# Performance work log

Hardware: AMD Instinct MI355X
Metric: run time of the kernel (lower is better)

The kernel has to match this reference:

```python
import jax, jax.numpy as jnp
import numpy as np

D, H, W, VP = 10, 400, 352, 35  # grid depth/height/width, points per voxel
C1_IN, C1_H = 7, 16   # VFE-1: Linear 7->16, concat -> 32
C2_IN, C2_H = 32, 64  # VFE-2: Linear 32->64, concat -> 128
BN_EPS = 1e-5


def setup_inputs() -> dict:
    key = jax.random.key(0)
    ks = jax.random.split(key, 12)
    K = 15000
    feature = jax.random.normal(ks[0], (K, VP, C1_IN), jnp.float32)
    keep = (jax.random.uniform(ks[1], (K, VP, 1)) < 0.8).astype(jnp.float32)
    feature = feature * keep
    bs = 1
    coordinate = jnp.concatenate([
        jax.random.randint(ks[2], (K, 1), 0, bs),
        jax.random.randint(ks[3], (K, 1), 0, D),
        jax.random.randint(ks[4], (K, 1), 0, H),
        jax.random.randint(ks[5], (K, 1), 0, W),
    ], axis=1).astype(jnp.int32)
    w1 = jax.random.normal(ks[6], (C1_IN, C1_H), jnp.float32) * 0.3
    b1 = jnp.zeros((C1_H,), jnp.float32)
    g1 = jnp.ones((C1_H,), jnp.float32)
    be1 = jnp.zeros((C1_H,), jnp.float32)
    w2 = jax.random.normal(ks[7], (C2_IN, C2_H), jnp.float32) * 0.15
    b2 = jnp.zeros((C2_H,), jnp.float32)
    g2 = jnp.ones((C2_H,), jnp.float32)
    be2 = jnp.zeros((C2_H,), jnp.float32)
    return dict(feature=feature, coordinate=coordinate, bs=bs,
                w1=w1, b1=b1, g1=g1, be1=be1,
                w2=w2, b2=b2, g2=g2, be2=be2)


def _vfe(x, mask, Wm, b, gamma, beta):
    # Linear + ReLU, then BatchNorm1d (training-mode batch stats over (K, VP))
    pw = jax.nn.relu(jnp.einsum('kpi,ih->kph', x, Wm) + b)
    mean = jnp.mean(pw, axis=(0, 1))
    var = jnp.var(pw, axis=(0, 1))  # biased variance, as BN uses for normalization
    pw = (pw - mean) * jax.lax.rsqrt(var + BN_EPS) * gamma + beta
    agg = jnp.max(pw, axis=1, keepdims=True)            # [K,1,Ch] per-voxel max
    concat = jnp.concatenate([pw, jnp.broadcast_to(agg, pw.shape)], axis=-1)
    return concat * mask                                  # mask broadcasts [K,VP,1]


def reference(feature, coordinate, bs, w1, b1, g1, be1, w2, b2, g2, be2):
    # mask: point is valid if max over its 7 features != 0
    mask = (jnp.max(feature, axis=2, keepdims=True) != 0).astype(feature.dtype)
    x = _vfe(feature, mask, w1, b1, g1, be1)   # [K,VP,32]
    x = _vfe(x, mask, w2, b2, g2, be2)         # [K,VP,128]
    voxelwise = jnp.max(x, axis=1)             # [K,128]
    c = coordinate
    out = jnp.zeros((bs, D, H, W, 2 * C2_H), feature.dtype)
    # sparse -> dense sums duplicate coordinates, matching torch.sparse to_dense
    out = out.at[c[:, 0], c[:, 1], c[:, 2], c[:, 3]].add(voxelwise)
    return out
```

## Files before the change

kernel.cpp:

```cpp
#include <hip/hip_runtime.h>
#include <math.h>

#define VPTS 35
#define CIN1 7
#define CH1  16
#define CH2  64
#define DD   10
#define HHH  400
#define WWW  352
#define BN_EPS 1e-5f
#define NSTRIPE 8


__global__ void k_init(float* __restrict__ ws) {
  for (int i = threadIdx.x; i < 1280; i += blockDim.x) ws[i] = 0.f;
}

__global__ void __launch_bounds__(256) k_A(
    const float* __restrict__ feat,
    const float* __restrict__ w1, const float* __restrict__ b1,
    float* __restrict__ red1p, float4* __restrict__ out4, long zA, int KP) {
  float w[CIN1][CH1], bb[CH1];
#pragma unroll
  for (int i = 0; i < CIN1; ++i)
#pragma unroll
    for (int c = 0; c < CH1; ++c) w[i][c] = w1[i * CH1 + c];
#pragma unroll
  for (int c = 0; c < CH1; ++c) bb[c] = b1[c];
  float s[CH1], q[CH1];
#pragma unroll
  for (int c = 0; c < CH1; ++c) { s[c] = 0.f; q[c] = 0.f; }
  int tid = blockIdx.x * blockDim.x + threadIdx.x;
  int stride = gridDim.x * blockDim.x;
  for (int idx = tid; idx < KP; idx += stride) {
    float x[CIN1];
#pragma unroll
    for (int i = 0; i < CIN1; ++i) x[i] = feat[(size_t)idx * CIN1 + i];
#pragma unroll
    for (int c = 0; c < CH1; ++c) {
      float a = bb[c];
#pragma unroll
      for (int i = 0; i < CIN1; ++i) a = fmaf(x[i], w[i][c], a);
      a = fmaxf(a, 0.f);
      s[c] += a;
      q[c] = fmaf(a, a, q[c]);
    }
  }
  float4 z = make_float4(0.f, 0.f, 0.f, 0.f);
  for (long i = tid; i < zA; i += stride) out4[i] = z;
  __shared__ float ssum[2 * CH1];
  if (threadIdx.x < 2 * CH1) ssum[threadIdx.x] = 0.f;
  __syncthreads();
#pragma unroll
  for (int c = 0; c < CH1; ++c) {
    float a = s[c], b = q[c];
    for (int o = 32; o > 0; o >>= 1) {
      a += __shfl_down(a, o);
      b += __shfl_down(b, o);
    }
    if ((threadIdx.x & 63) == 0) {
      atomicAdd(&ssum[c], a);
      atomicAdd(&ssum[CH1 + c], b);
    }
  }
  __syncthreads();
  if (threadIdx.x < 2 * CH1)
    atomicAdd(&red1p[(blockIdx.x & (NSTRIPE - 1)) * 2 * CH1 + threadIdx.x],
              ssum[threadIdx.x]);
}

__global__ void __launch_bounds__(256) k_heavy(
    const float* __restrict__ feat,
    const float* __restrict__ w1, const float* __restrict__ b1,
    const float* __restrict__ g1, const float* __restrict__ be1,
    const float* __restrict__ red1p,
    const float* __restrict__ w2, const float* __restrict__ b2,
    const float* __restrict__ g2,
    float* __restrict__ red2p,
    float* __restrict__ E1buf, float* __restrict__ E2buf,
    float* __restrict__ FLbuf, int K,
    float4* __restrict__ out4, long z0, long n4, float invN) {
  __shared__ __align__(16) float fs_s[4][248];
  __shared__ __align__(16) float pw1_s[4][560];
  __shared__ __align__(16) float agg1_s[4][16];
  __shared__ float ss[2 * CH2];
  int t = threadIdx.x, lane = t & 63, w = t >> 6;
  float* fs   = fs_s[w];
  float* pw1  = pw1_s[w];
  float* agg1 = agg1_s[w];

  int c1 = lane & 15;
  float r1s = 0.f, r1q = 0.f;
#pragma unroll
  for (int sIdx = 0; sIdx < NSTRIPE; ++sIdx) {
    r1s += red1p[sIdx * 2 * CH1 + c1];
    r1q += red1p[sIdx * 2 * CH1 + CH1 + c1];
  }
  float mean1 = r1s * invN;
  float var1  = r1q * invN - mean1 * mean1;
  float sc1   = g1[c1] * rsqrtf(var1 + BN_EPS);
  float sh1   = be1[c1] - mean1 * sc1;
  float b1c   = b1[c1];
  float w1r[CIN1];
#pragma unroll
  for (int j = 0; j < CIN1; ++j) w1r[j] = w1[j * CH1 + c1];
  float wcol[32];
#pragma unroll
  for (int i = 0; i < 32; ++i) wcol[i] = w2[i * CH2 + lane];
  float b2c = b2[lane];
  float sgn = (g2[lane] >= 0.f) ? 1.f : -1.f;

  float lsum = 0.f, lsq = 0.f;
  int waveg = blockIdx.x * 4 + w;
  int nwave = gridDim.x * 4;
  long zstride = (long)gridDim.x * 256;
  long zi = z0 + (long)blockIdx.x * 256 + t;
  float4 zv = make_float4(0.f, 0.f, 0.f, 0.f);
  for (int k = waveg; k < K; k += nwave) {
    for (int i = lane; i < VPTS * CIN1; i += 64)
      fs[i] = feat[(size_t)k * (VPTS * CIN1) + i];
    bool vbit = false;
    if (lane < VPTS) {
      float m = fs[lane * CIN1];
#pragma unroll
      for (int j = 1; j < CIN1; ++j) m = fmaxf(m, fs[lane * CIN1 + j]);
      vbit = (m != 0.f);
    }
    unsigned long long mbits = __ballot(vbit);
#pragma unroll
    for (int j = 0; j < 9; ++j) {
      int idx = lane + 64 * j;
      if (idx < VPTS * CH1) {
        int p = idx >> 4;
        float a = b1c;
#pragma unroll
        for (int jj = 0; jj < CIN1; ++jj) a = fmaf(fs[p * CIN1 + jj], w1r[jj], a);
        a = fmaxf(a, 0.f);
        pw1[idx] = fmaf(a, sc1, sh1);
      }
    }
    {
      int g = lane >> 4;
      float am = -INFINITY;
      for (int p = g; p < VPTS; p += 4) am = fmaxf(am, pw1[p * CH1 + c1]);
      am = fmaxf(am, __shfl_xor(am, 16));
      am = fmaxf(am, __shfl_xor(am, 32));
      if (lane < CH1) agg1[lane] = am;
    }
#pragma unroll
    for (int u = 0; u < 20; ++u) {
      if (zi < n4) { out4[zi] = zv; zi += zstride; }
    }
    float aggdot = 0.f;
    {
      const float4* a4 = (const float4*)agg1;
#pragma unroll
      for (int i = 0; i < 4; ++i) {
        float4 v = a4[i];
        aggdot = fmaf(v.x, wcol[16 + 4 * i + 0], aggdot);
        aggdot = fmaf(v.y, wcol[16 + 4 * i + 1], aggdot);
        aggdot = fmaf(v.z, wcol[16 + 4 * i + 2], aggdot);
        aggdot = fmaf(v.w, wcol[16 + 4 * i + 3], aggdot);
      }
    }
    float E1w = -INFINITY, E2w = -INFINITY;
    const float4* p4 = (const float4*)pw1;
    for (int p = 0; p < VPTS; ++p) {
      float4 v0 = p4[p * 4 + 0], v1 = p4[p * 4 + 1];
      float4 v2 = p4[p * 4 + 2], v3 = p4[p * 4 + 3];
      float low = 0.f;
      low = fmaf(v0.x, wcol[0], low);  low = fmaf(v0.y, wcol[1], low);
      low = fmaf(v0.z, wcol[2], low);  low = fmaf(v0.w, wcol[3], low);
      low = fmaf(v1.x, wcol[4], low);  low = fmaf(v1.y, wcol[5], low);
      low = fmaf(v1.z, wcol[6], low);  low = fmaf(v1.w, wcol[7], low);
      low = fmaf(v2.x, wcol[8], low);  low = fmaf(v2.y, wcol[9], low);
      low = fmaf(v2.z, wcol[10], low); low = fmaf(v2.w, wcol[11], low);
      low = fmaf(v3.x, wcol[12], low); low = fmaf(v3.y, wcol[13], low);
      low = fmaf(v3.z, wcol[14], low); low = fmaf(v3.w, wcol[15], low);
      bool valid = (mbits >> p) & 1ull;
      float m = valid ? 1.f : 0.f;
      float pw2 = fmaxf(fmaf(m, low + aggdot, b2c), 0.f);
      lsum += pw2;
      lsq = fmaf(pw2, pw2, lsq);
      float sp = sgn * pw2;
      E2w = fmaxf(E2w, sp);
      if (valid) E1w = fmaxf(E1w, sp);
    }
    E1buf[(size_t)k * 64 + lane] = E1w;
    E2buf[(size_t)k * 64 + lane] = E2w;
    if (lane == 0) FLbuf[k] = (float)__popcll(mbits);
  }
  for (; zi < n4; zi += zstride) out4[zi] = zv;
  if (t < 2 * CH2) ss[t] = 0.f;
  __syncthreads();
  atomicAdd(&ss[lane], lsum);
  atomicAdd(&ss[CH2 + lane], lsq);
  __syncthreads();
  if (t < 2 * CH2)
    atomicAdd(&red2p[(blockIdx.x & (NSTRIPE - 1)) * 2 * CH2 + t], ss[t]);
}

__global__ void __launch_bounds__(256) k_scatter(
    const float* __restrict__ E1buf, const float* __restrict__ E2buf,
    const float* __restrict__ FLbuf, const float* __restrict__ red2p,
    const float* __restrict__ g2, const float* __restrict__ be2,
    const int* __restrict__ coord, float* __restrict__ out, int K,
    float invN) {
  __shared__ float scsh2_s[2 * CH2];
  int t = threadIdx.x;
  if (t < CH2) {
    float rs = 0.f, rq = 0.f;
#pragma unroll
    for (int sIdx = 0; sIdx < NSTRIPE; ++sIdx) {
      rs += red2p[sIdx * 2 * CH2 + t];
      rq += red2p[sIdx * 2 * CH2 + CH2 + t];
    }
    float mean = rs * invN;
    float var = rq * invN - mean * mean;
    float inv = rsqrtf(var + BN_EPS);
    float sc = g2[t] * inv;
    scsh2_s[t] = sc;
    scsh2_s[CH2 + t] = be2[t] - mean * sc;
  }
  __syncthreads();
  int k = blockIdx.x * 2 + (t >> 7);
  if (k >= K) return;
  int tl = t & 127;
  int c = tl & 63;
  float nv = FLbuf[k];
  bool anyV = nv > 0.f;
  bool anyI = nv < (float)VPTS;
  float sc = scsh2_s[c], sh = scsh2_s[CH2 + c];
  float cand = -INFINITY;
  if (anyV) {
    float E = (tl < 64) ? E1buf[(size_t)k * 64 + c] : E2buf[(size_t)k * 64 + c];
    cand = fmaf(fabsf(sc), E, sh);
  }
  if (anyI) cand = fmaxf(cand, 0.f);
  int4 cc = *reinterpret_cast<const int4*>(coord + (size_t)k * 4);
  long vox = ((long)(cc.x * DD + cc.y) * HHH + cc.z) * WWW + cc.w;
  atomicAdd(&out[vox * (2 * CH2) + tl], cand);
}

__global__ void __launch_bounds__(256) k_zero(float4* __restrict__ out4,
                                              long n4, float* __restrict__ wsfb) {
  long i = (long)blockIdx.x * blockDim.x + threadIdx.x;
  long stride = (long)gridDim.x * blockDim.x;
  float4 z = make_float4(0.f, 0.f, 0.f, 0.f);
  for (; i < n4; i += stride) out4[i] = z;
  if (blockIdx.x == 0 && threadIdx.x < 320) wsfb[threadIdx.x] = 0.f;
}

__global__ void k_finalize(const float* __restrict__ red,
                           const float* __restrict__ g,
                           const float* __restrict__ be,
                           float* __restrict__ scsh, int CH, float invN) {
  int c = threadIdx.x;
  if (c < CH) {
    float mean = red[c] * invN;
    float var = red[CH + c] * invN - mean * mean;
    float inv = rsqrtf(var + BN_EPS);
    float sc = g[c] * inv;
    scsh[c] = sc;
    scsh[CH + c] = be[c] - mean * sc;
  }
}

__global__ void __launch_bounds__(256) k_stats1_fb(
    const float* __restrict__ feat,
    const float* __restrict__ w1, const float* __restrict__ b1,
    float* __restrict__ red1, int KP) {
  float w[CIN1][CH1], bb[CH1];
#pragma unroll
  for (int i = 0; i < CIN1; ++i)
#pragma unroll
    for (int c = 0; c < CH1; ++c) w[i][c] = w1[i * CH1 + c];
#pragma unroll
  for (int c = 0; c < CH1; ++c) bb[c] = b1[c];
  float s[CH1], q[CH1];
#pragma unroll
  for (int c = 0; c < CH1; ++c) { s[c] = 0.f; q[c] = 0.f; }
  int tid = blockIdx.x * blockDim.x + threadIdx.x;
  int stride = gridDim.x * blockDim.x;
  for (int idx = tid; idx < KP; idx += stride) {
    float x[CIN1];
#pragma unroll
    for (int i = 0; i < CIN1; ++i) x[i] = feat[(size_t)idx * CIN1 + i];
#pragma unroll
    for (int c = 0; c < CH1; ++c) {
      float a = bb[c];
#pragma unroll
      for (int i = 0; i < CIN1; ++i) a = fmaf(x[i], w[i][c], a);
      a = fmaxf(a, 0.f);
      s[c] += a;
      q[c] = fmaf(a, a, q[c]);
    }
  }
  __shared__ float ssum[2 * CH1];
  if (threadIdx.x < 2 * CH1) ssum[threadIdx.x] = 0.f;
  __syncthreads();
#pragma unroll
  for (int c = 0; c < CH1; ++c) {
    float a = s[c], b = q[c];
    for (int o = 32; o > 0; o >>= 1) {
      a += __shfl_down(a, o);
      b += __shfl_down(b, o);
    }
    if ((threadIdx.x & 63) == 0) {
      atomicAdd(&ssum[c], a);
      atomicAdd(&ssum[CH1 + c], b);
    }
  }
  __syncthreads();
  if (threadIdx.x < 2 * CH1) atomicAdd(&red1[threadIdx.x], ssum[threadIdx.x]);
}

__device__ __forceinline__ void compute_x2_old(
    const float* __restrict__ feat, int k, int t,
    const float* __restrict__ w1, const float* __restrict__ b1,
    const float* __restrict__ scsh1,
    float* fs, float* mask_s, float* pw1_s, float* agg1_s, float* x2_s) {
  if (t < VPTS * CIN1) fs[t] = feat[(size_t)k * (VPTS * CIN1) + t];
  __syncthreads();
  if (t < VPTS) {
    float m = fs[t * CIN1];
#pragma unroll
    for (int i = 1; i < CIN1; ++i) m = fmaxf(m, fs[t * CIN1 + i]);
    mask_s[t] = (m != 0.f) ? 1.f : 0.f;
  }
  for (int i = t; i < VPTS * CH1; i += 256) {
    int p = i >> 4, c = i & 15;
    float acc = b1[c];
#pragma unroll
    for (int j = 0; j < CIN1; ++j) acc = fmaf(fs[p * CIN1 + j], w1[j * CH1 + c], acc);
    acc = fmaxf(acc, 0.f);
    pw1_s[i] = fmaf(acc, scsh1[c], scsh1[CH1 + c]);
  }
  __syncthreads();
  if (t < CH1) {
    float m = pw1_s[t];
    for (int p = 1; p < VPTS; ++p) m = fmaxf(m, pw1_s[p * CH1 + t]);
    agg1_s[t] = m;
  }
  __syncthreads();
  for (int i = t; i < VPTS * 32; i += 256) {
    int p = i >> 5, c = i & 31;
    x2_s[i] = (c < CH1 ? pw1_s[p * CH1 + c] : agg1_s[c - CH1]) * mask_s[p];
  }
  __syncthreads();
}

__global__ void __launch_bounds__(256) k_stats2_old(
    const float* __restrict__ feat,
    const float* __restrict__ w1, const float* __restrict__ b1,
    const float* __restrict__ scsh1,
    const float* __restrict__ w2, const float* __restrict__ b2,
    float* __restrict__ red2, int K) {
  __shared__ float fs[VPTS * CIN1], mask_s[VPTS], pw1_s[VPTS * CH1], agg1_s[CH1];
  __shared__ __align__(16) float x2_s[VPTS * 32];
  __shared__ __align__(16) float w2_s[32 * CH2];
  __shared__ float ss[2 * CH2];
  int t = threadIdx.x;
  for (int i = t; i < 32 * CH2; i += 256) w2_s[i] = w2[i];
  if (t < 2 * CH2) ss[t] = 0.f;
  __syncthreads();
  int c = t & 63;
  float wcol[32];
#pragma unroll
  for (int i = 0; i < 32; ++i) wcol[i] = w2_s[i * CH2 + c];
  float bb = b2[c];
  float lsum = 0.f, lsq = 0.f;
  for (int k = blockIdx.x; k < K; k += gridDim.x) {
    compute_x2_old(feat, k, t, w1, b1, scsh1, fs, mask_s, pw1_s, agg1_s, x2_s);
    for (int p = t >> 6; p < VPTS; p += 4) {
      const float4* xv = (const float4*)(x2_s + p * 32);
      float a = bb;
#pragma unroll
      for (int i = 0; i < 8; ++i) {
        float4 v = xv[i];
        a = fmaf(v.x, wcol[4 * i + 0], a);
        a = fmaf(v.y, wcol[4 * i + 1], a);
        a = fmaf(v.z, wcol[4 * i + 2], a);
        a = fmaf(v.w, wcol[4 * i + 3], a);
      }
      a = fmaxf(a, 0.f);
      lsum += a;
      lsq = fmaf(a, a, lsq);
    }
  }
  atomicAdd(&ss[c], lsum);
  atomicAdd(&ss[CH2 + c], lsq);
  __syncthreads();
  if (t < 2 * CH2) atomicAdd(&red2[t], ss[t]);
}

__global__ void __launch_bounds__(256) k_final_old(
    const float* __restrict__ feat,
    const float* __restrict__ w1, const float* __restrict__ b1,
    const float* __restrict__ scsh1,
    const float* __restrict__ w2, const float* __restrict__ b2,
    const float* __restrict__ scsh2,
    const int* __restrict__ coord,
    float* __restrict__ out, int K) {
  __shared__ float fs[VPTS * CIN1], mask_s[VPTS], pw1_s[VPTS * CH1], agg1_s[CH1];
  __shared__ __align__(16) float x2_s[VPTS * 32];
  __shared__ __align__(16) float w2_s[32 * CH2];
  __shared__ float pw2_s[VPTS * CH2];
  __shared__ float agg2_s[CH2];
  int t = threadIdx.x;
  for (int i = t; i < 32 * CH2; i += 256) w2_s[i] = w2[i];
  __syncthreads();
  int c = t & 63;
  float wcol[32];
#pragma unroll
  for (int i = 0; i < 32; ++i) wcol[i] = w2_s[i * CH2 + c];
  float bb = b2[c];
  float sc = scsh2[c], sh = scsh2[CH2 + c];
  for (int k = blockIdx.x; k < K; k += gridDim.x) {
    compute_x2_old(feat, k, t, w1, b1, scsh1, fs, mask_s, pw1_s, agg1_s, x2_s);
    for (int p = t >> 6; p < VPTS; p += 4) {
      const float4* xv = (const float4*)(x2_s + p * 32);
      float a = bb;
#pragma unroll
      for (int i = 0; i < 8; ++i) {
        float4 v = xv[i];
        a = fmaf(v.x, wcol[4 * i + 0], a);
        a = fmaf(v.y, wcol[4 * i + 1], a);
        a = fmaf(v.z, wcol[4 * i + 2], a);
        a = fmaf(v.w, wcol[4 * i + 3], a);
      }
      a = fmaxf(a, 0.f);
      pw2_s[p * CH2 + c] = fmaf(a, sc, sh);
    }
    __syncthreads();
    if (t < CH2) {
      float m = pw2_s[t];
      for (int p = 1; p < VPTS; ++p) m = fmaxf(m, pw2_s[p * CH2 + t]);
      agg2_s[t] = m;
    }
    __syncthreads();
    if (t < 2 * CH2) {
      float vm = -INFINITY;
      if (t < CH2) {
        for (int p = 0; p < VPTS; ++p) vm = fmaxf(vm, pw2_s[p * CH2 + t] * mask_s[p]);
      } else {
        float a = agg2_s[t - CH2];
        for (int p = 0; p < VPTS; ++p) vm = fmaxf(vm, a * mask_s[p]);
      }
      int4 cc = *reinterpret_cast<const int4*>(coord + (size_t)k * 4);
      long vox = ((long)(cc.x * DD + cc.y) * HHH + cc.z) * WWW + cc.w;
      atomicAdd(&out[vox * (2 * CH2) + t], vm);
    }
  }
}

extern "C" void kernel_launch(void* const* d_in, const int* in_sizes, int n_in,
                              void* d_out, int out_size, void* d_ws, size_t ws_size,
                              hipStream_t stream) {
  const float* feat = (const float*)d_in[0];
  const int* coord  = (const int*)d_in[1];
  const float* w1  = (const float*)d_in[3];
  const float* b1  = (const float*)d_in[4];
  const float* g1  = (const float*)d_in[5];
  const float* be1 = (const float*)d_in[6];
  const float* w2  = (const float*)d_in[7];
  const float* b2  = (const float*)d_in[8];
  const float* g2  = (const float*)d_in[9];
  const float* be2 = (const float*)d_in[10];
  float* out = (float*)d_out;
  float* ws = (float*)d_ws;

  int K = in_sizes[0] / (VPTS * CIN1);
  int KP = K * VPTS;
  float invN = 1.f / (float)KP;

  float* red1p = ws;
  float* red2p = ws + 256;
  float* fb    = ws + 1280;
  float* E1buf = ws + 2048;
  float* E2buf = E1buf + (size_t)64 * K;
  float* FLbuf = E2buf + (size_t)64 * K;

  size_t need_bytes = (2048 + (size_t)K * 129) * sizeof(float);

  long n4 = (long)out_size / 4;
  long zA = (n4 * 55) / 100;

  if (ws_size >= need_bytes) {
    k_init<<<1, 1024, 0, stream>>>(ws);
    k_A<<<2048, 256, 0, stream>>>(feat, w1, b1, red1p, (float4*)out, zA, KP);
    k_heavy<<<2048, 256, 0, stream>>>(feat, w1, b1, g1, be1, red1p,
                                      w2, b2, g2, red2p, E1buf, E2buf, FLbuf, K,
                                      (float4*)out, zA, n4, invN);
    k_scatter<<<(K + 1) / 2, 256, 0, stream>>>(E1buf, E2buf, FLbuf, red2p,
                                               g2, be2, coord, out, K, invN);
  } else {
    float* red1  = fb;
    float* scsh1 = fb + 32;
    float* red2  = fb + 64;
    float* scsh2 = fb + 192;
    k_zero<<<2048, 256, 0, stream>>>((float4*)out, n4, fb);
    k_stats1_fb<<<512, 256, 0, stream>>>(feat, w1, b1, red1, KP);
    k_finalize<<<1, 64, 0, stream>>>(red1, g1, be1, scsh1, CH1, invN);
    k_stats2_old<<<1024, 256, 0, stream>>>(feat, w1, b1, scsh1, w2, b2, red2, K);
    k_finalize<<<1, 64, 0, stream>>>(red2, g2, be2, scsh2, CH2, invN);
    k_final_old<<<2048, 256, 0, stream>>>(feat, w1, b1, scsh1, w2, b2, scsh2,
                                          coord, out, K);
  }
}
```

Baseline: 194.4 us.

## Fuse pipeline into one cooperative kernel with grid syncs and role-split blocks

Replaces the init/stats/heavy/scatter launch chain with a single cooperative kernel that uses grid.sync between phases. In each phase some blocks compute (BN1 stats, then VFE-2) while the rest zero the output buffer. This removes launch gaps and the workspace init kernel. The cost is fewer blocks (capped by occupancy at 1024), fewer waves doing the heavy VFE work, and the overhead of grid-wide barriers.

Measured after the change: 432.9 us. +122.7%, slower.

```diff
diff --git a/kernel.cpp b/kernel.cpp
--- a/kernel.cpp
+++ b/kernel.cpp
@@ -1,5 +1,8 @@
 #include <hip/hip_runtime.h>
+#include <hip/hip_cooperative_groups.h>
 #include <math.h>
+
+namespace cg = cooperative_groups;
 
 #define VPTS 35
 #define CIN1 7
@@ -12,8 +15,233 @@
 #define NSTRIPE 8
 
 
+__global__ void __launch_bounds__(256, 4) k_fused(
+    const float* __restrict__ feat, const int* __restrict__ coord,
+    const float* __restrict__ w1, const float* __restrict__ b1,
+    const float* __restrict__ g1, const float* __restrict__ be1,
+    const float* __restrict__ w2, const float* __restrict__ b2,
+    const float* __restrict__ g2, const float* __restrict__ be2,
+    float* __restrict__ out, float* __restrict__ ws,
+    int K, int KP, long n4, long f1, float invN) {
+  cg::grid_group grid = cg::this_grid();
+  float4* out4 = (float4*)out;
+  float* ws1   = ws;
+  float* red2p = ws + 2048;
+  float* E1buf = ws + 4096;
+  float* E2buf = E1buf + (size_t)64 * K;
+  float* FLbuf = E2buf + (size_t)64 * K;
+
+  const int G  = gridDim.x;
+  const int Sb = G >> 4;
+  const int Hb = G >> 1;
+  const int t = threadIdx.x, lane = t & 63, w = t >> 6;
+
+  __shared__ __align__(16) float fs_s[4][248];
+  __shared__ __align__(16) float pw1_s[4][560];
+  __shared__ __align__(16) float agg1_s[4][16];
+  __shared__ float ss[2 * CH2];
+  __shared__ float ls[2 * CH1];
+  __shared__ float scsh2_s[2 * CH2];
+
+  if (blockIdx.x < Sb) {
+    int tp = blockIdx.x * 256 + t;
+    int p0 = tp >> 2, cq = tp & 3;
+    int pstride = Sb * 64;
+    float w1q[CIN1][4], b1q[4], s[4], q[4];
+#pragma unroll
+    for (int j = 0; j < CIN1; ++j)
+#pragma unroll
+      for (int cc = 0; cc < 4; ++cc) w1q[j][cc] = w1[j * CH1 + cq * 4 + cc];
+#pragma unroll
+    for (int cc = 0; cc < 4; ++cc) {
+      b1q[cc] = b1[cq * 4 + cc];
+      s[cc] = 0.f; q[cc] = 0.f;
+    }
+    for (int p = p0; p < KP; p += pstride) {
+      float x[CIN1];
+#pragma unroll
+      for (int j = 0; j < CIN1; ++j) x[j] = feat[(size_t)p * CIN1 + j];
+#pragma unroll
+      for (int cc = 0; cc < 4; ++cc) {
+        float a = b1q[cc];
+#pragma unroll
+        for (int j = 0; j < CIN1; ++j) a = fmaf(x[j], w1q[j][cc], a);
+        a = fmaxf(a, 0.f);
+        s[cc] += a;
+        q[cc] = fmaf(a, a, q[cc]);
+      }
+    }
+    if (t < 2 * CH1) ls[t] = 0.f;
+    __syncthreads();
+#pragma unroll
+    for (int cc = 0; cc < 4; ++cc) {
+      atomicAdd(&ls[cq * 4 + cc], s[cc]);
+      atomicAdd(&ls[CH1 + cq * 4 + cc], q[cc]);
+    }
+    __syncthreads();
+    if (t < 2 * CH1) ws1[blockIdx.x * 32 + t] = ls[t];
+  } else {
+    if (blockIdx.x == G - 1) {
+      for (int i = t; i < NSTRIPE * 2 * CH2; i += 256) red2p[i] = 0.f;
+    }
+    float4 zv = make_float4(0.f, 0.f, 0.f, 0.f);
+    long fb = G - Sb;
+    long stride = fb * 256;
+    for (long zi = (long)(blockIdx.x - Sb) * 256 + t; zi < f1; zi += stride)
+      out4[zi] = zv;
+  }
+  grid.sync();
+
+  if (blockIdx.x < Hb) {
+    float* fs   = fs_s[w];
+    float* pw1  = pw1_s[w];
+    float* agg1 = agg1_s[w];
+    int c1 = lane & 15;
+    float r1s = 0.f, r1q = 0.f;
+    for (int sIdx = 0; sIdx < Sb; ++sIdx) {
+      r1s += ws1[sIdx * 32 + c1];
+      r1q += ws1[sIdx * 32 + CH1 + c1];
+    }
+    float mean1 = r1s * invN;
+    float var1  = r1q * invN - mean1 * mean1;
+    float sc1   = g1[c1] * rsqrtf(var1 + BN_EPS);
+    float sh1   = be1[c1] - mean1 * sc1;
+    float b1c   = b1[c1];
+    float w1r[CIN1];
+#pragma unroll
+    for (int j = 0; j < CIN1; ++j) w1r[j] = w1[j * CH1 + c1];
+    float wcol[32];
+#pragma unroll
+    for (int i = 0; i < 32; ++i) wcol[i] = w2[i * CH2 + lane];
+    float b2c = b2[lane];
+    float sgn = (g2[lane] >= 0.f) ? 1.f : -1.f;
+
+    float lsum = 0.f, lsq = 0.f;
+    int waveg = blockIdx.x * 4 + w;
+    int nwave = Hb * 4;
+    for (int k = waveg; k < K; k += nwave) {
+      for (int i = lane; i < VPTS * CIN1; i += 64)
+        fs[i] = feat[(size_t)k * (VPTS * CIN1) + i];
+      bool vbit = false;
+      if (lane < VPTS) {
+        float m = fs[lane * CIN1];
+#pragma unroll
+        for (int j = 1; j < CIN1; ++j) m = fmaxf(m, fs[lane * CIN1 + j]);
+        vbit = (m != 0.f);
+      }
+      unsigned long long mbits = __ballot(vbit);
+#pragma unroll
+      for (int j = 0; j < 9; ++j) {
+        int idx = lane + 64 * j;
+        if (idx < VPTS * CH1) {
+          int p = idx >> 4;
+          float a = b1c;
+#pragma unroll
+          for (int jj = 0; jj < CIN1; ++jj)
+            a = fmaf(fs[p * CIN1 + jj], w1r[jj], a);
+          a = fmaxf(a, 0.f);
+          pw1[idx] = fmaf(a, sc1, sh1);
+        }
+      }
+      {
+        int g = lane >> 4;
+        float am = -INFINITY;
+        for (int p = g; p < VPTS; p += 4) am = fmaxf(am, pw1[p * CH1 + c1]);
+        am = fmaxf(am, __shfl_xor(am, 16));
+        am = fmaxf(am, __shfl_xor(am, 32));
+        if (lane < CH1) agg1[lane] = am;
+      }
+      float aggdot = 0.f;
+      {
+        const float4* a4 = (const float4*)agg1;
+#pragma unroll
+        for (int i = 0; i < 4; ++i) {
+          float4 v = a4[i];
+          aggdot = fmaf(v.x, wcol[16 + 4 * i + 0], aggdot);
+          aggdot = fmaf(v.y, wcol[16 + 4 * i + 1], aggdot);
+          aggdot = fmaf(v.z, wcol[16 + 4 * i + 2], aggdot);
+          aggdot = fmaf(v.w, wcol[16 + 4 * i + 3], aggdot);
+        }
+      }
+      float E1w = -INFINITY, E2w = -INFINITY;
+      const float4* p4 = (const float4*)pw1;
+      for (int p = 0; p < VPTS; ++p) {
+        float4 v0 = p4[p * 4 + 0], v1 = p4[p * 4 + 1];
+        float4 v2 = p4[p * 4 + 2], v3 = p4[p * 4 + 3];
+        float low = 0.f;
+        low = fmaf(v0.x, wcol[0], low);  low = fmaf(v0.y, wcol[1], low);
+        low = fmaf(v0.z, wcol[2], low);  low = fmaf(v0.w, wcol[3], low);
+        low = fmaf(v1.x, wcol[4], low);  low = fmaf(v1.y, wcol[5], low);
+        low = fmaf(v1.z, wcol[6], low);  low = fmaf(v1.w, wcol[7], low);
+        low = fmaf(v2.x, wcol[8], low);  low = fmaf(v2.y, wcol[9], low);
+        low = fmaf(v2.z, wcol[10], low); low = fmaf(v2.w, wcol[11], low);
+        low = fmaf(v3.x, wcol[12], low); low = fmaf(v3.y, wcol[13], low);
+        low = fmaf(v3.z, wcol[14], low); low = fmaf(v3.w, wcol[15], low);
+        bool valid = (mbits >> p) & 1ull;
+        float m = valid ? 1.f : 0.f;
+        float pw2 = fmaxf(fmaf(m, low + aggdot, b2c), 0.f);
+        lsum += pw2;
+        lsq = fmaf(pw2, pw2, lsq);
+        float sp = sgn * pw2;
+        E2w = fmaxf(E2w, sp);
+        if (valid) E1w = fmaxf(E1w, sp);
+      }
+      E1buf[(size_t)k * 64 + lane] = E1w;
+      E2buf[(size_t)k * 64 + lane] = E2w;
+      if (lane == 0) FLbuf[k] = (float)__popcll(mbits);
+    }
+    if (t < 2 * CH2) ss[t] = 0.f;
+    __syncthreads();
+    atomicAdd(&ss[lane], lsum);
+    atomicAdd(&ss[CH2 + lane], lsq);
+    __syncthreads();
+    if (t < 2 * CH2)
+      atomicAdd(&red2p[(blockIdx.x & (NSTRIPE - 1)) * 2 * CH2 + t], ss[t]);
+  } else {
+    float4 zv = make_float4(0.f, 0.f, 0.f, 0.f);
+    long fb = G - Hb;
+    long stride = fb * 256;
+    for (long zi = f1 + (long)(blockIdx.x - Hb) * 256 + t; zi < n4; zi += stride)
+      out4[zi] = zv;
+  }
+  grid.sync();
+
+  if (t < CH2) {
+    float rs = 0.f, rq = 0.f;
+#pragma unroll
+    for (int sIdx = 0; sIdx < NSTRIPE; ++sIdx) {
+      rs += red2p[sIdx * 2 * CH2 + t];
+      rq += red2p[sIdx * 2 * CH2 + CH2 + t];
+    }
+    float mean = rs * invN;
+    float var = rq * invN - mean * mean;
+    float inv = rsqrtf(var + BN_EPS);
+    float sc = g2[t] * inv;
+    scsh2_s[t] = sc;
+    scsh2_s[CH2 + t] = be2[t] - mean * sc;
+  }
+  __syncthreads();
+  int tl = t & 127;
+  int c = tl & 63;
+  float sc = scsh2_s[c], sh = scsh2_s[CH2 + c];
+  for (int k = blockIdx.x * 2 + (t >> 7); k < K; k += G * 2) {
+    float nv = FLbuf[k];
+    bool anyV = nv > 0.f;
+    bool anyI = nv < (float)VPTS;
+    float cand = -INFINITY;
+    if (anyV) {
+      float E = (tl < 64) ? E1buf[(size_t)k * 64 + c] : E2buf[(size_t)k * 64 + c];
+      cand = fmaf(fabsf(sc), E, sh);
+    }
+    if (anyI) cand = fmaxf(cand, 0.f);
+    int4 cc = *reinterpret_cast<const int4*>(coord + (size_t)k * 4);
+    long vox = ((long)(cc.x * DD + cc.y) * HHH + cc.z) * WWW + cc.w;
+    atomicAdd(&out[vox * (2 * CH2) + tl], cand);
+  }
+}
+
 __global__ void k_init(float* __restrict__ ws) {
-  for (int i = threadIdx.x; i < 1280; i += blockDim.x) ws[i] = 0.f;
+  for (int i = threadIdx.x; i < 3392; i += blockDim.x) ws[i] = 0.f;
 }
 
 __global__ void __launch_bounds__(256) k_A(
@@ -69,7 +297,7 @@
               ssum[threadIdx.x]);
 }
 
-__global__ void __launch_bounds__(256) k_heavy(
+__global__ void __launch_bounds__(256) k_heavy_fb(
     const float* __restrict__ feat,
     const float* __restrict__ w1, const float* __restrict__ b1,
     const float* __restrict__ g1, const float* __restrict__ be1,
@@ -88,7 +316,6 @@
   float* fs   = fs_s[w];
   float* pw1  = pw1_s[w];
   float* agg1 = agg1_s[w];
-
   int c1 = lane & 15;
   float r1s = 0.f, r1q = 0.f;
 #pragma unroll
@@ -109,13 +336,9 @@
   for (int i = 0; i < 32; ++i) wcol[i] = w2[i * CH2 + lane];
   float b2c = b2[lane];
   float sgn = (g2[lane] >= 0.f) ? 1.f : -1.f;
-
   float lsum = 0.f, lsq = 0.f;
   int waveg = blockIdx.x * 4 + w;
   int nwave = gridDim.x * 4;
-  long zstride = (long)gridDim.x * 256;
-  long zi = z0 + (long)blockIdx.x * 256 + t;
-  float4 zv = make_float4(0.f, 0.f, 0.f, 0.f);
   for (int k = waveg; k < K; k += nwave) {
     for (int i = lane; i < VPTS * CIN1; i += 64)
       fs[i] = feat[(size_t)k * (VPTS * CIN1) + i];
@@ -146,10 +369,6 @@
       am = fmaxf(am, __shfl_xor(am, 16));
       am = fmaxf(am, __shfl_xor(am, 32));
       if (lane < CH1) agg1[lane] = am;
-    }
-#pragma unroll
-    for (int u = 0; u < 20; ++u) {
-      if (zi < n4) { out4[zi] = zv; zi += zstride; }
     }
     float aggdot = 0.f;
     {
@@ -190,7 +409,12 @@
     E2buf[(size_t)k * 64 + lane] = E2w;
     if (lane == 0) FLbuf[k] = (float)__popcll(mbits);
   }
-  for (; zi < n4; zi += zstride) out4[zi] = zv;
+  {
+    float4 zv = make_float4(0.f, 0.f, 0.f, 0.f);
+    long stride = (long)gridDim.x * 256;
+    for (long zi = z0 + (long)blockIdx.x * 256 + t; zi < n4; zi += stride)
+      out4[zi] = zv;
+  }
   if (t < 2 * CH2) ss[t] = 0.f;
   __syncthreads();
   atomicAdd(&ss[lane], lsum);
@@ -200,7 +424,7 @@
     atomicAdd(&red2p[(blockIdx.x & (NSTRIPE - 1)) * 2 * CH2 + t], ss[t]);
 }
 
-__global__ void __launch_bounds__(256) k_scatter(
+__global__ void __launch_bounds__(256) k_scatter_fb(
     const float* __restrict__ E1buf, const float* __restrict__ E2buf,
     const float* __restrict__ FLbuf, const float* __restrict__ red2p,
     const float* __restrict__ g2, const float* __restrict__ be2,
@@ -240,218 +464,6 @@
   int4 cc = *reinterpret_cast<const int4*>(coord + (size_t)k * 4);
   long vox = ((long)(cc.x * DD + cc.y) * HHH + cc.z) * WWW + cc.w;
   atomicAdd(&out[vox * (2 * CH2) + tl], cand);
-}
-
-__global__ void __launch_bounds__(256) k_zero(float4* __restrict__ out4,
-                                              long n4, float* __restrict__ wsfb) {
-  long i = (long)blockIdx.x * blockDim.x + threadIdx.x;
-  long stride = (long)gridDim.x * blockDim.x;
-  float4 z = make_float4(0.f, 0.f, 0.f, 0.f);
-  for (; i < n4; i += stride) out4[i] = z;
-  if (blockIdx.x == 0 && threadIdx.x < 320) wsfb[threadIdx.x] = 0.f;
-}
-
-__global__ void k_finalize(const float* __restrict__ red,
-                           const float* __restrict__ g,
-                           const float* __restrict__ be,
-                           float* __restrict__ scsh, int CH, float invN) {
-  int c = threadIdx.x;
-  if (c < CH) {
-    float mean = red[c] * invN;
-    float var = red[CH + c] * invN - mean * mean;
-    float inv = rsqrtf(var + BN_EPS);
-    float sc = g[c] * inv;
-    scsh[c] = sc;
-    scsh[CH + c] = be[c] - mean * sc;
-  }
-}
-
-__global__ void __launch_bounds__(256) k_stats1_fb(
-    const float* __restrict__ feat,
-    const float* __restrict__ w1, const float* __restrict__ b1,
-    float* __restrict__ red1, int KP) {
-  float w[CIN1][CH1], bb[CH1];
-#pragma unroll
-  for (int i = 0; i < CIN1; ++i)
-#pragma unroll
-    for (int c = 0; c < CH1; ++c) w[i][c] = w1[i * CH1 + c];
-#pragma unroll
-  for (int c = 0; c < CH1; ++c) bb[c] = b1[c];
-  float s[CH1], q[CH1];
-#pragma unroll
-  for (int c = 0; c < CH1; ++c) { s[c] = 0.f; q[c] = 0.f; }
-  int tid = blockIdx.x * blockDim.x + threadIdx.x;
-  int stride = gridDim.x * blockDim.x;
-  for (int idx = tid; idx < KP; idx += stride) {
-    float x[CIN1];
-#pragma unroll
-    for (int i = 0; i < CIN1; ++i) x[i] = feat[(size_t)idx * CIN1 + i];
-#pragma unroll
-    for (int c = 0; c < CH1; ++c) {
-      float a = bb[c];
-#pragma unroll
-      for (int i = 0; i < CIN1; ++i) a = fmaf(x[i], w[i][c], a);
-      a = fmaxf(a, 0.f);
-      s[c] += a;
-      q[c] = fmaf(a, a, q[c]);
-    }
-  }
-  __shared__ float ssum[2 * CH1];
-  if (threadIdx.x < 2 * CH1) ssum[threadIdx.x] = 0.f;
-  __syncthreads();
-#pragma unroll
-  for (int c = 0; c < CH1; ++c) {
-    float a = s[c], b = q[c];
-    for (int o = 32; o > 0; o >>= 1) {
-      a += __shfl_down(a, o);
-      b += __shfl_down(b, o);
-    }
-    if ((threadIdx.x & 63) == 0) {
-      atomicAdd(&ssum[c], a);
-      atomicAdd(&ssum[CH1 + c], b);
-    }
-  }
-  __syncthreads();
-  if (threadIdx.x < 2 * CH1) atomicAdd(&red1[threadIdx.x], ssum[threadIdx.x]);
-}
-
-__device__ __forceinline__ void compute_x2_old(
-    const float* __restrict__ feat, int k, int t,
-    const float* __restrict__ w1, const float* __restrict__ b1,
-    const float* __restrict__ scsh1,
-    float* fs, float* mask_s, float* pw1_s, float* agg1_s, float* x2_s) {
-  if (t < VPTS * CIN1) fs[t] = feat[(size_t)k * (VPTS * CIN1) + t];
-  __syncthreads();
-  if (t < VPTS) {
-    float m = fs[t * CIN1];
-#pragma unroll
-    for (int i = 1; i < CIN1; ++i) m = fmaxf(m, fs[t * CIN1 + i]);
-    mask_s[t] = (m != 0.f) ? 1.f : 0.f;
-  }
-  for (int i = t; i < VPTS * CH1; i += 256) {
-    int p = i >> 4, c = i & 15;
-    float acc = b1[c];
-#pragma unroll
-    for (int j = 0; j < CIN1; ++j) acc = fmaf(fs[p * CIN1 + j], w1[j * CH1 + c], acc);
-    acc = fmaxf(acc, 0.f);
-    pw1_s[i] = fmaf(acc, scsh1[c], scsh1[CH1 + c]);
-  }
-  __syncthreads();
-  if (t < CH1) {
-    float m = pw1_s[t];
-    for (int p = 1; p < VPTS; ++p) m = fmaxf(m, pw1_s[p * CH1 + t]);
-    agg1_s[t] = m;
-  }
-  __syncthreads();
-  for (int i = t; i < VPTS * 32; i += 256) {
-    int p = i >> 5, c = i & 31;
-    x2_s[i] = (c < CH1 ? pw1_s[p * CH1 + c] : agg1_s[c - CH1]) * mask_s[p];
-  }
-  __syncthreads();
-}
-
-__global__ void __launch_bounds__(256) k_stats2_old(
-    const float* __restrict__ feat,
-    const float* __restrict__ w1, const float* __restrict__ b1,
-    const float* __restrict__ scsh1,
-    const float* __restrict__ w2, const float* __restrict__ b2,
-    float* __restrict__ red2, int K) {
-  __shared__ float fs[VPTS * CIN1], mask_s[VPTS], pw1_s[VPTS * CH1], agg1_s[CH1];
-  __shared__ __align__(16) float x2_s[VPTS * 32];
-  __shared__ __align__(16) float w2_s[32 * CH2];
-  __shared__ float ss[2 * CH2];
-  int t = threadIdx.x;
-  for (int i = t; i < 32 * CH2; i += 256) w2_s[i] = w2[i];
-  if (t < 2 * CH2) ss[t] = 0.f;
-  __syncthreads();
-  int c = t & 63;
-  float wcol[32];
-#pragma unroll
-  for (int i = 0; i < 32; ++i) wcol[i] = w2_s[i * CH2 + c];
-  float bb = b2[c];
-  float lsum = 0.f, lsq = 0.f;
-  for (int k = blockIdx.x; k < K; k += gridDim.x) {
-    compute_x2_old(feat, k, t, w1, b1, scsh1, fs, mask_s, pw1_s, agg1_s, x2_s);
-    for (int p = t >> 6; p < VPTS; p += 4) {
-      const float4* xv = (const float4*)(x2_s + p * 32);
-      float a = bb;
-#pragma unroll
-      for (int i = 0; i < 8; ++i) {
-        float4 v = xv[i];
-        a = fmaf(v.x, wcol[4 * i + 0], a);
-        a = fmaf(v.y, wcol[4 * i + 1], a);
-        a = fmaf(v.z, wcol[4 * i + 2], a);
-        a = fmaf(v.w, wcol[4 * i + 3], a);
-      }
-      a = fmaxf(a, 0.f);
-      lsum += a;
-      lsq = fmaf(a, a, lsq);
-    }
-  }
-  atomicAdd(&ss[c], lsum);
-  atomicAdd(&ss[CH2 + c], lsq);
-  __syncthreads();
-  if (t < 2 * CH2) atomicAdd(&red2[t], ss[t]);
-}
-
-__global__ void __launch_bounds__(256) k_final_old(
-    const float* __restrict__ feat,
-    const float* __restrict__ w1, const float* __restrict__ b1,
-    const float* __restrict__ scsh1,
-    const float* __restrict__ w2, const float* __restrict__ b2,
-    const float* __restrict__ scsh2,
-    const int* __restrict__ coord,
-    float* __restrict__ out, int K) {
-  __shared__ float fs[VPTS * CIN1], mask_s[VPTS], pw1_s[VPTS * CH1], agg1_s[CH1];
-  __shared__ __align__(16) float x2_s[VPTS * 32];
-  __shared__ __align__(16) float w2_s[32 * CH2];
-  __shared__ float pw2_s[VPTS * CH2];
-  __shared__ float agg2_s[CH2];
-  int t = threadIdx.x;
-  for (int i = t; i < 32 * CH2; i += 256) w2_s[i] = w2[i];
-  __syncthreads();
-  int c = t & 63;
-  float wcol[32];
-#pragma unroll
-  for (int i = 0; i < 32; ++i) wcol[i] = w2_s[i * CH2 + c];
-  float bb = b2[c];
-  float sc = scsh2[c], sh = scsh2[CH2 + c];
-  for (int k = blockIdx.x; k < K; k += gridDim.x) {
-    compute_x2_old(feat, k, t, w1, b1, scsh1, fs, mask_s, pw1_s, agg1_s, x2_s);
-    for (int p = t >> 6; p < VPTS; p += 4) {
-      const float4* xv = (const float4*)(x2_s + p * 32);
-      float a = bb;
-#pragma unroll
-      for (int i = 0; i < 8; ++i) {
-        float4 v = xv[i];
-        a = fmaf(v.x, wcol[4 * i + 0], a);
-        a = fmaf(v.y, wcol[4 * i + 1], a);
-        a = fmaf(v.z, wcol[4 * i + 2], a);
-        a = fmaf(v.w, wcol[4 * i + 3], a);
-      }
-      a = fmaxf(a, 0.f);
-      pw2_s[p * CH2 + c] = fmaf(a, sc, sh);
-    }
-    __syncthreads();
-    if (t < CH2) {
-      float m = pw2_s[t];
-      for (int p = 1; p < VPTS; ++p) m = fmaxf(m, pw2_s[p * CH2 + t]);
-      agg2_s[t] = m;
-    }
-    __syncthreads();
-    if (t < 2 * CH2) {
-      float vm = -INFINITY;
-      if (t < CH2) {
-        for (int p = 0; p < VPTS; ++p) vm = fmaxf(vm, pw2_s[p * CH2 + t] * mask_s[p]);
-      } else {
-        float a = agg2_s[t - CH2];
-        for (int p = 0; p < VPTS; ++p) vm = fmaxf(vm, a * mask_s[p]);
-      }
-      int4 cc = *reinterpret_cast<const int4*>(coord + (size_t)k * 4);
-      long vox = ((long)(cc.x * DD + cc.y) * HHH + cc.z) * WWW + cc.w;
-      atomicAdd(&out[vox * (2 * CH2) + t], vm);
-    }
-  }
 }
 
 extern "C" void kernel_launch(void* const* d_in, const int* in_sizes, int n_in,
@@ -474,37 +486,43 @@
   int KP = K * VPTS;
   float invN = 1.f / (float)KP;
 
-  float* red1p = ws;
-  float* red2p = ws + 256;
-  float* fb    = ws + 1280;
-  float* E1buf = ws + 2048;
-  float* E2buf = E1buf + (size_t)64 * K;
-  float* FLbuf = E2buf + (size_t)64 * K;
-
-  size_t need_bytes = (2048 + (size_t)K * 129) * sizeof(float);
-
+  size_t need_bytes = (4096 + (size_t)K * 129) * sizeof(float);
   long n4 = (long)out_size / 4;
-  long zA = (n4 * 55) / 100;
-
+  long f1 = (n4 * 3) / 10;
+
+  bool done = false;
   if (ws_size >= need_bytes) {
+    int maxB = 0;
+    hipError_t oe = hipOccupancyMaxActiveBlocksPerMultiprocessor(
+        &maxB, k_fused, 256, 0);
+    if (oe == hipSuccess && maxB >= 1) {
+      int G = maxB * 256;
+      if (G > 1024) G = 1024;
+      if (G >= 64) {
+        void* args[] = {(void*)&feat, (void*)&coord, (void*)&w1, (void*)&b1,
+                        (void*)&g1, (void*)&be1, (void*)&w2, (void*)&b2,
+                        (void*)&g2, (void*)&be2, (void*)&out, (void*)&ws,
+                        (void*)&K, (void*)&KP, (void*)&n4, (void*)&f1,
+                        (void*)&invN};
+        hipError_t le = hipLaunchCooperativeKernel(
+            (const void*)k_fused, dim3(G), dim3(256), args, 0, stream);
+        if (le == hipSuccess) done = true;
+      }
+    }
+  }
+  if (!done && ws_size >= need_bytes) {
+    float* red1p = ws;
+    float* red2p = ws + 2048;
+    float* E1buf = ws + 4096;
+    float* E2buf = E1buf + (size_t)64 * K;
+    float* FLbuf = E2buf + (size_t)64 * K;
+    long zA = (n4 * 55) / 100;
     k_init<<<1, 1024, 0, stream>>>(ws);
     k_A<<<2048, 256, 0, stream>>>(feat, w1, b1, red1p, (float4*)out, zA, KP);
-    k_heavy<<<2048, 256, 0, stream>>>(feat, w1, b1, g1, be1, red1p,
-                                      w2, b2, g2, red2p, E1buf, E2buf, FLbuf, K,
-                                      (float4*)out, zA, n4, invN);
-    k_scatter<<<(K + 1) / 2, 256, 0, stream>>>(E1buf, E2buf, FLbuf, red2p,
-                                               g2, be2, coord, out, K, invN);
-  } else {
-    float* red1  = fb;
-    float* scsh1 = fb + 32;
-    float* red2  = fb + 64;
-    float* scsh2 = fb + 192;
-    k_zero<<<2048, 256, 0, stream>>>((float4*)out, n4, fb);
-    k_stats1_fb<<<512, 256, 0, stream>>>(feat, w1, b1, red1, KP);
-    k_finalize<<<1, 64, 0, stream>>>(red1, g1, be1, scsh1, CH1, invN);
-    k_stats2_old<<<1024, 256, 0, stream>>>(feat, w1, b1, scsh1, w2, b2, red2, K);
-    k_finalize<<<1, 64, 0, stream>>>(red2, g2, be2, scsh2, CH2, invN);
-    k_final_old<<<2048, 256, 0, stream>>>(feat, w1, b1, scsh1, w2, b2, scsh2,
-                                          coord, out, K);
+    k_heavy_fb<<<2048, 256, 0, stream>>>(feat, w1, b1, g1, be1, red1p,
+                                         w2, b2, g2, red2p, E1buf, E2buf,
+                                         FLbuf, K, (float4*)out, zA, n4, invN);
+    k_scatter_fb<<<(K + 1) / 2, 256, 0, stream>>>(E1buf, E2buf, FLbuf, red2p,
+                                                  g2, be2, coord, out, K, invN);
   }
 }
```
